# Kernel tuning notes

Hardware: AMD Instinct MI355X
Metric: run time of the kernel (lower is better)

The kernel has to match this reference:

```python
import jax, jax.numpy as jnp
import numpy as np

VOCAB, X, H, C_CLS = 32000, 300, 512, 5
B, N_LEAVES = 256, 256  # complete binary trees, depth 9, 511 nodes/tree

def setup_inputs() -> dict:
    key = jax.random.key(0)
    ks = jax.random.split(key, 10)
    s = lambda k, shp, fan: jax.random.normal(k, shp, jnp.float32) * (1.0 / np.sqrt(fan))
    return {
        'wordid': jax.random.randint(ks[0], (B, N_LEAVES), 0, VOCAB),
        'emb': jax.random.normal(ks[1], (VOCAB, X), jnp.float32) * 0.1,
        'W_iou_w': s(ks[2], (3 * H, X), X),
        'W_iou_b': jnp.zeros((3 * H,), jnp.float32),
        'U_iou_w': s(ks[3], (3 * H, 2 * H), 2 * H),
        'U_iou_b': jnp.zeros((3 * H,), jnp.float32),
        'U_f_w': s(ks[4], (2 * H, 2 * H), 2 * H),
        'U_f_b': jnp.zeros((2 * H,), jnp.float32),
        'lin_w': s(ks[5], (C_CLS, H), H),
        'lin_b': jnp.zeros((C_CLS,), jnp.float32),
    }

def _cell(iou, c_f):
    i, o, u = jnp.split(iou, 3, axis=-1)
    c = jax.nn.sigmoid(i) * jnp.tanh(u) + c_f
    h = jax.nn.sigmoid(o) * jnp.tanh(c)
    return h, c

def reference(wordid, emb, W_iou_w, W_iou_b, U_iou_w, U_iou_b, U_f_w, U_f_b, lin_w, lin_b):
    b, n = wordid.shape
    # leaves: is_leaf=1 -> iou = W_iou(x), c_f = 0
    x = emb[wordid]                                   # [B, L, X]
    iou = x @ W_iou_w.T + W_iou_b                     # [B, L, 3H]
    h, c = _cell(iou, 0.0)
    hs = [h]
    # internal levels: reduce over exactly 2 children (binary TreeLSTM)
    while h.shape[1] > 1:
        m = h.shape[1] // 2
        h_cat = h.reshape(b, m, 2 * H)                # concat of 2 children
        c_pair = c.reshape(b, m, 2, H)
        f = jax.nn.sigmoid(h_cat @ U_f_w.T + U_f_b).reshape(b, m, 2, H)
        c_f = jnp.sum(f * c_pair, axis=2)             # [B, m, H]
        iou = h_cat @ U_iou_w.T + U_iou_b             # is_leaf=0 branch
        h, c = _cell(iou, c_f)
        hs.append(h)
    h_all = jnp.concatenate(hs, axis=1)               # [B, 2L-1, H], leaves-first topo order
    # dropout is identity at inference
    logits = h_all @ lin_w.T + lin_b                  # [B, 2L-1, num_classes]
    return logits
```

## Files before the change

kernel.cpp:

```cpp
#include <hip/hip_runtime.h>
#include <hip/hip_bf16.h>


typedef __bf16 bf16;
typedef bf16  bf16x8 __attribute__((ext_vector_type(8)));
typedef float f32x4  __attribute__((ext_vector_type(4)));

__device__ __forceinline__ float sigm(float x){ return 1.0f/(1.0f + __expf(-x)); }
__device__ __forceinline__ float tanh_f(float x){ return 1.0f - 2.0f/(__expf(2.0f*x)+1.0f); }

__device__ __forceinline__ void gload16(const bf16* g, bf16* l){
  __builtin_amdgcn_global_load_lds(
      (const __attribute__((address_space(1))) void*)g,
      (__attribute__((address_space(3))) void*)l, 16, 0, 0);
}

#define FENCE_VM(N) do{ asm volatile("s_waitcnt vmcnt(" #N ")" ::: "memory"); \
  __builtin_amdgcn_sched_barrier(0); __builtin_amdgcn_s_barrier(); \
  __builtin_amdgcn_sched_barrier(0); }while(0)
#define FENCE_LGKM do{ asm volatile("s_waitcnt lgkmcnt(0)" ::: "memory"); \
  __builtin_amdgcn_sched_barrier(0); __builtin_amdgcn_s_barrier(); \
  __builtin_amdgcn_sched_barrier(0); }while(0)

__global__ void cvt_all(const float* __restrict__ Wiou, const float* __restrict__ Uiou,
                        const float* __restrict__ Uf, const float* __restrict__ emb,
                        bf16* __restrict__ Wpad, bf16* __restrict__ Uall,
                        bf16* __restrict__ embp){
  const long long gid = (long long)blockIdx.x*256 + threadIdx.x;
  const long long NW = 122880, NE = 2560000, NU = 655360;
  if (gid < NW + NE){
    long long g = gid;
    const float* src; bf16* dst;
    if (g < NW){ src = Wiou; dst = Wpad; }
    else       { g -= NW; src = emb; dst = embp; }
    const int r = (int)(g / 80), v = (int)(g % 80);
    bf16 o0, o1, o2, o3;
    if (v < 75){
      const f32x4 x = *(const f32x4*)(src + (size_t)r*300 + v*4);
      o0=(bf16)x[0]; o1=(bf16)x[1]; o2=(bf16)x[2]; o3=(bf16)x[3];
    } else {
      o0=o1=o2=o3=(bf16)0.f;
    }
    bf16* d = dst + (size_t)r*320 + v*4;
    d[0]=o0; d[1]=o1; d[2]=o2; d[3]=o3;
  } else {
    const long long i4 = gid - NW - NE;
    if (i4 < NU){
      const size_t i = (size_t)i4*4;
      const float* s = (i < (size_t)1536*1024) ? (Uiou + i)
                                               : (Uf + (i - (size_t)1536*1024));
      const f32x4 x = *(const f32x4*)s;
      bf16* d = Uall + i;
      d[0]=(bf16)x[0]; d[1]=(bf16)x[1]; d[2]=(bf16)x[2]; d[3]=(bf16)x[3];
    }
  }
}

__global__ __launch_bounds__(256, 2)
void leaf128_kernel(const int* __restrict__ wordid, const bf16* __restrict__ embp,
                    const bf16* __restrict__ Wpad, const float* __restrict__ Wb,
                    bf16* __restrict__ hcur, float* __restrict__ ccur)
{
  __shared__ bf16 lsA[2][128*32];
  __shared__ bf16 lsB[2][192*32];
  const int t = threadIdx.x;
  const int mrow0 = blockIdx.x*128, nblk = blockIdx.y*64;
  const int lane16 = t&15, quad = (t&63)>>4, w = t>>6;

  const int lrow = t>>2;
  const int qsw  = ((t&3) ^ ((t>>3)&3))*8;
  const int wb   = (t & 192)*8;

  const int wid0 = wordid[mrow0 + lrow];
  const int wid1 = wordid[mrow0 + 64 + lrow];
  const bf16* srcA0 = embp + (size_t)wid0*320 + qsw;
  const bf16* srcA1 = embp + (size_t)wid1*320 + qsw;
  const bf16* srcB0 = Wpad + (size_t)(0*512 + nblk + lrow)*320 + qsw;
  const bf16* srcB1 = Wpad + (size_t)(1*512 + nblk + lrow)*320 + qsw;
  const bf16* srcB2 = Wpad + (size_t)(2*512 + nblk + lrow)*320 + qsw;

  const int sA   = (t>>1)&3;
  const int aoff = lane16*32 + ((quad ^ sA)*8);
  const int boff = (w*16 + lane16)*32 + ((quad ^ sA)*8);

  f32x4 acc[3][8];
  const f32x4 zero = {0.f,0.f,0.f,0.f};
  #pragma unroll
  for(int o=0;o<3;o++){
    #pragma unroll
    for(int rt=0;rt<8;rt++) acc[o][rt]=zero;
  }

  {
    gload16(srcA0     , lsA[0] + wb);        gload16(srcA1     , lsA[0] + 2048 + wb);
    gload16(srcB0     , lsB[0] + wb);        gload16(srcB1     , lsB[0] + 2048 + wb);
    gload16(srcB2     , lsB[0] + 4096 + wb);
    gload16(srcA0 + 32, lsA[1] + wb);        gload16(srcA1 + 32, lsA[1] + 2048 + wb);
    gload16(srcB0 + 32, lsB[1] + wb);        gload16(srcB1 + 32, lsB[1] + 2048 + wb);
    gload16(srcB2 + 32, lsB[1] + 4096 + wb);
  }
  FENCE_VM(5);

  for (int ks = 0; ks < 10; ks++){
    const int cur = ks & 1;
    bf16x8 bfrag[3], afrag[8];
    #pragma unroll
    for(int g=0;g<3;g++) bfrag[g] = *(const bf16x8*)&lsB[cur][g*2048 + boff];
    #pragma unroll
    for(int rt=0;rt<8;rt++) afrag[rt] = *(const bf16x8*)&lsA[cur][rt*512 + aoff];
    FENCE_LGKM;
    if (ks < 8){
      const int k0 = (ks+2)*32;
      gload16(srcA0 + k0, lsA[cur] + wb);        gload16(srcA1 + k0, lsA[cur] + 2048 + wb);
      gload16(srcB0 + k0, lsB[cur] + wb);        gload16(srcB1 + k0, lsB[cur] + 2048 + wb);
      gload16(srcB2 + k0, lsB[cur] + 4096 + wb);
    }
    __builtin_amdgcn_s_setprio(1);
    #pragma unroll
    for(int rt=0;rt<8;rt++){
      #pragma unroll
      for(int g=0;g<3;g++)
        acc[g][rt] = __builtin_amdgcn_mfma_f32_16x16x32_bf16(afrag[rt], bfrag[g], acc[g][rt], 0,0,0);
    }
    __builtin_amdgcn_s_setprio(0);
    if (ks < 8)      FENCE_VM(5);
    else if (ks < 9) FENCE_VM(0);
  }
  const int j = nblk + w*16 + lane16;
  const float bi=Wb[j], bo=Wb[512+j], bu=Wb[1024+j];
  #pragma unroll
  for(int rt=0;rt<8;rt++){
    #pragma unroll
    for(int reg=0;reg<4;reg++){
      const int row = mrow0 + rt*16 + quad*4 + reg;
      float iv=acc[0][rt][reg]+bi, ov=acc[1][rt][reg]+bo, uv=acc[2][rt][reg]+bu;
      float c = sigm(iv)*tanh_f(uv);
      float h = sigm(ov)*tanh_f(c);
      ccur[(size_t)row*512 + j] = c;
      hcur[(size_t)row*512 + j] = (bf16)h;
    }
  }
}

__global__ __launch_bounds__(256, 3)
void level_kernel(const bf16* __restrict__ hprev, bf16* __restrict__ hcur,
                  const float* __restrict__ cprev, float* __restrict__ ccur,
                  const bf16* __restrict__ Uall, const float* __restrict__ Uioub,
                  const float* __restrict__ Ufb)
{
  __shared__ bf16 lsA[2][64*32];
  __shared__ bf16 lsB[2][320*32];
  const int t = threadIdx.x;
  const int mrow0 = blockIdx.x*64, nblk = blockIdx.y*64;
  const int lane16 = t&15, quad = (t&63)>>4, w = t>>6;

  const int lrow = t>>2;
  const int qsw  = ((t&3) ^ ((t>>3)&3))*8;
  const int wb   = (t & 192)*8;

  const bf16* srcA0 = hprev + (size_t)(mrow0 + lrow)*1024 + qsw;
  const bf16* srcB0 = Uall + (size_t)(0*512 + nblk + lrow)*1024 + qsw;
  const bf16* srcB1 = Uall + (size_t)(1*512 + nblk + lrow)*1024 + qsw;
  const bf16* srcB2 = Uall + (size_t)(2*512 + nblk + lrow)*1024 + qsw;
  const bf16* srcB3 = Uall + (size_t)(3*512 + nblk + lrow)*1024 + qsw;
  const bf16* srcB4 = Uall + (size_t)(4*512 + nblk + lrow)*1024 + qsw;

  const int sA   = (t>>1)&3;
  const int aoff = lane16*32 + ((quad ^ sA)*8);
  const int boff = (w*16 + lane16)*32 + ((quad ^ sA)*8);

#define LV64_DMA(buf, k0) do{ \
  gload16(srcA0 + (k0), lsA[buf] + wb); \
  gload16(srcB0 + (k0), lsB[buf] + wb);        gload16(srcB1 + (k0), lsB[buf] + 2048 + wb); \
  gload16(srcB2 + (k0), lsB[buf] + 4096 + wb); gload16(srcB3 + (k0), lsB[buf] + 6144 + wb); \
  gload16(srcB4 + (k0), lsB[buf] + 8192 + wb); }while(0)

  f32x4 acc[5][4];
  const f32x4 zero = {0.f,0.f,0.f,0.f};
  #pragma unroll
  for(int o=0;o<5;o++){
    #pragma unroll
    for(int rt=0;rt<4;rt++) acc[o][rt]=zero;
  }

  LV64_DMA(0, 0); LV64_DMA(1, 32);
  FENCE_VM(6);

  for (int ks = 0; ks < 32; ks++){
    const int cur = ks & 1;
    bf16x8 bfrag[5], afrag[4];
    #pragma unroll
    for(int g=0;g<5;g++) bfrag[g] = *(const bf16x8*)&lsB[cur][g*2048 + boff];
    #pragma unroll
    for(int rt=0;rt<4;rt++) afrag[rt] = *(const bf16x8*)&lsA[cur][rt*512 + aoff];
    FENCE_LGKM;
    if (ks < 30){
      LV64_DMA(cur, (ks+2)*32);
    }
    __builtin_amdgcn_s_setprio(1);
    #pragma unroll
    for(int rt=0;rt<4;rt++){
      #pragma unroll
      for(int g=0;g<5;g++)
        acc[g][rt] = __builtin_amdgcn_mfma_f32_16x16x32_bf16(afrag[rt], bfrag[g], acc[g][rt], 0,0,0);
    }
    __builtin_amdgcn_s_setprio(0);
    if (ks < 30)       FENCE_VM(6);
    else if (ks < 31)  FENCE_VM(0);
  }

  const int j = nblk + w*16 + lane16;
  const float bi =Uioub[j], bo=Uioub[512+j], bu=Uioub[1024+j];
  const float bfl=Ufb[j],   bfr=Ufb[512+j];
  #pragma unroll
  for(int rt=0;rt<4;rt++){
    #pragma unroll
    for(int reg=0;reg<4;reg++){
      const int row = mrow0 + rt*16 + quad*4 + reg;
      float iv=acc[0][rt][reg]+bi, ov=acc[1][rt][reg]+bo, uv=acc[2][rt][reg]+bu;
      float fl=acc[3][rt][reg]+bfl, fr=acc[4][rt][reg]+bfr;
      float cl = cprev[((size_t)row*2  )*512 + j];
      float cr = cprev[((size_t)row*2+1)*512 + j];
      float cf = sigm(fl)*cl + sigm(fr)*cr;
      float c  = sigm(iv)*tanh_f(uv) + cf;
      float h  = sigm(ov)*tanh_f(c);
      ccur[(size_t)row*512 + j] = c;
      hcur[(size_t)row*512 + j] = (bf16)h;
    }
  }
#undef LV64_DMA
}

__global__ __launch_bounds__(256, 2)
void level128_kernel(const bf16* __restrict__ hprev, bf16* __restrict__ hcur,
                     const float* __restrict__ cprev, float* __restrict__ ccur,
                     const bf16* __restrict__ Uall, const float* __restrict__ Uioub,
                     const float* __restrict__ Ufb)
{
  __shared__ bf16 lsA[128*32];
  __shared__ bf16 lsB[2][320*32];
  const int t = threadIdx.x;
  const int mrow0 = blockIdx.x*128, nblk = blockIdx.y*64;
  const int lane16 = t&15, quad = (t&63)>>4, w = t>>6;

  const int lrow = t>>2;
  const int qsw  = ((t&3) ^ ((t>>3)&3))*8;
  const int wb   = (t & 192)*8;

  const bf16* srcA0 = hprev + (size_t)(mrow0 + lrow)*1024 + qsw;
  const bf16* srcA1 = hprev + (size_t)(mrow0 + 64 + lrow)*1024 + qsw;
  const bf16* srcB0 = Uall + (size_t)(0*512 + nblk + lrow)*1024 + qsw;
  const bf16* srcB1 = Uall + (size_t)(1*512 + nblk + lrow)*1024 + qsw;
  const bf16* srcB2 = Uall + (size_t)(2*512 + nblk + lrow)*1024 + qsw;
  const bf16* srcB3 = Uall + (size_t)(3*512 + nblk + lrow)*1024 + qsw;
  const bf16* srcB4 = Uall + (size_t)(4*512 + nblk + lrow)*1024 + qsw;

  const int sA   = (t>>1)&3;
  const int aoff = lane16*32 + ((quad ^ sA)*8);
  const int boff = (w*16 + lane16)*32 + ((quad ^ sA)*8);

#define LVL_DMA_A(k0) do{ \
  gload16(srcA0 + (k0), lsA + wb);             gload16(srcA1 + (k0), lsA + 2048 + wb); }while(0)
#define LVL_DMA_B(buf, k0) do{ \
  gload16(srcB0 + (k0), lsB[buf] + wb);        gload16(srcB1 + (k0), lsB[buf] + 2048 + wb); \
  gload16(srcB2 + (k0), lsB[buf] + 4096 + wb); gload16(srcB3 + (k0), lsB[buf] + 6144 + wb); \
  gload16(srcB4 + (k0), lsB[buf] + 8192 + wb); }while(0)

  f32x4 acc[5][8];
  const f32x4 zero = {0.f,0.f,0.f,0.f};
  #pragma unroll
  for(int o=0;o<5;o++){
    #pragma unroll
    for(int rt=0;rt<8;rt++) acc[o][rt]=zero;
  }

  LVL_DMA_A(0); LVL_DMA_B(0, 0);
  LVL_DMA_B(1, 32);
  FENCE_VM(5);

  for (int ks = 0; ks < 32; ks++){
    const int cur = ks & 1;
    bf16x8 bfrag[5], afrag[8];
    #pragma unroll
    for(int g=0;g<5;g++) bfrag[g] = *(const bf16x8*)&lsB[cur][g*2048 + boff];
    #pragma unroll
    for(int rt=0;rt<8;rt++) afrag[rt] = *(const bf16x8*)&lsA[rt*512 + aoff];
    FENCE_LGKM;
    if (ks < 31) LVL_DMA_A(ks*32 + 32);
    if (ks < 30) LVL_DMA_B(cur, (ks+2)*32);
    __builtin_amdgcn_s_setprio(1);
    #pragma unroll
    for(int rt=0;rt<8;rt++){
      #pragma unroll
      for(int g=0;g<5;g++)
        acc[g][rt] = __builtin_amdgcn_mfma_f32_16x16x32_bf16(afrag[rt], bfrag[g], acc[g][rt], 0,0,0);
    }
    __builtin_amdgcn_s_setprio(0);
    if (ks < 30)       FENCE_VM(5);
    else if (ks < 31)  FENCE_VM(0);
  }

  const int j = nblk + w*16 + lane16;
  const float bi =Uioub[j], bo=Uioub[512+j], bu=Uioub[1024+j];
  const float bfl=Ufb[j],   bfr=Ufb[512+j];
  #pragma unroll
  for(int rt=0;rt<8;rt++){
    #pragma unroll
    for(int reg=0;reg<4;reg++){
      const int row = mrow0 + rt*16 + quad*4 + reg;
      float iv=acc[0][rt][reg]+bi, ov=acc[1][rt][reg]+bo, uv=acc[2][rt][reg]+bu;
      float fl=acc[3][rt][reg]+bfl, fr=acc[4][rt][reg]+bfr;
      float cl = cprev[((size_t)row*2  )*512 + j];
      float cr = cprev[((size_t)row*2+1)*512 + j];
      float cf = sigm(fl)*cl + sigm(fr)*cr;
      float c  = sigm(iv)*tanh_f(uv) + cf;
      float h  = sigm(ov)*tanh_f(c);
      ccur[(size_t)row*512 + j] = c;
      hcur[(size_t)row*512 + j] = (bf16)h;
    }
  }
#undef LVL_DMA_A
#undef LVL_DMA_B
}

__global__ __launch_bounds__(256)
void logits_kernel(const bf16* __restrict__ h, const float* __restrict__ linw,
                   const float* __restrict__ linb, float* __restrict__ out,
                   int rowbase, int lgm, int mask, int off){
  const int row = blockIdx.x*4 + (threadIdx.x>>6);
  const int l = threadIdx.x & 63;
  bf16x8 hv = *(const bf16x8*)(h + (size_t)row*512 + l*8);
  float hf[8];
  #pragma unroll
  for(int jj=0;jj<8;jj++) hf[jj] = (float)hv[jj];
  float s[5];
  #pragma unroll
  for(int c=0;c<5;c++){
    const f32x4 w0 = *(const f32x4*)(linw + c*512 + l*8);
    const f32x4 w1 = *(const f32x4*)(linw + c*512 + l*8 + 4);
    float a = 0.f;
    #pragma unroll
    for(int jj=0;jj<4;jj++) a += hf[jj]*w0[jj] + hf[4+jj]*w1[jj];
    s[c]=a;
  }
  #pragma unroll
  for(int o=32;o>0;o>>=1){
    #pragma unroll
    for(int c=0;c<5;c++) s[c] += __shfl_down(s[c], o, 64);
  }
  if (l==0){
    const int g = rowbase + row;
    const int node = (g>>lgm)*511 + off + (g&mask);
    #pragma unroll
    for(int c=0;c<5;c++) out[(size_t)node*5+c] = s[c] + linb[c];
  }
}

__global__ __launch_bounds__(256)
void logits2_kernel(const bf16* __restrict__ ha, int rows_a, int lgm_a, int mask_a, int off_a,
                    const bf16* __restrict__ hb, int lgm_b, int mask_b, int off_b,
                    const float* __restrict__ linw, const float* __restrict__ linb,
                    float* __restrict__ out){
  const int row = blockIdx.x*4 + (threadIdx.x>>6);
  const int l = threadIdx.x & 63;
  const bf16* hrow; int g, lgm, mask, off;
  if (row < rows_a){ hrow = ha + (size_t)row*512;            g = row;           lgm=lgm_a; mask=mask_a; off=off_a; }
  else             { hrow = hb + (size_t)(row-rows_a)*512;   g = row - rows_a;  lgm=lgm_b; mask=mask_b; off=off_b; }
  bf16x8 hv = *(const bf16x8*)(hrow + l*8);
  float hf[8];
  #pragma unroll
  for(int jj=0;jj<8;jj++) hf[jj] = (float)hv[jj];
  float s[5];
  #pragma unroll
  for(int c=0;c<5;c++){
    const f32x4 w0 = *(const f32x4*)(linw + c*512 + l*8);
    const f32x4 w1 = *(const f32x4*)(linw + c*512 + l*8 + 4);
    float a = 0.f;
    #pragma unroll
    for(int jj=0;jj<4;jj++) a += hf[jj]*w0[jj] + hf[4+jj]*w1[jj];
    s[c]=a;
  }
  #pragma unroll
  for(int o=32;o>0;o>>=1){
    #pragma unroll
    for(int c=0;c<5;c++) s[c] += __shfl_down(s[c], o, 64);
  }
  if (l==0){
    const int node = (g>>lgm)*511 + off + (g&mask);
    #pragma unroll
    for(int c=0;c<5;c++) out[(size_t)node*5+c] = s[c] + linb[c];
  }
}

__global__ void zero_out(float* out, int n){
  int i = blockIdx.x*256 + threadIdx.x;
  if (i < n) out[i] = 0.f;
}

extern "C" void kernel_launch(void* const* d_in, const int* in_sizes, int n_in,
                              void* d_out, int out_size, void* d_ws, size_t ws_size,
                              hipStream_t stream)
{
  const int*   wordid = (const int*)d_in[0];
  const float* emb    = (const float*)d_in[1];
  const float* Wiou   = (const float*)d_in[2];
  const float* Wioub  = (const float*)d_in[3];
  const float* Uiou   = (const float*)d_in[4];
  const float* Uioub  = (const float*)d_in[5];
  const float* Uf     = (const float*)d_in[6];
  const float* Ufb    = (const float*)d_in[7];
  const float* linw   = (const float*)d_in[8];
  const float* linb   = (const float*)d_in[9];
  float* out = (float*)d_out;

  const size_t oWPD  = 0;
  const size_t oUALL = oWPD  + (size_t)1536*320*2;
  const size_t oEMB  = oUALL + (size_t)2560*1024*2;
  const size_t oH1   = oEMB  + (size_t)32000*320*2;
  const size_t oC1   = oH1   + (size_t)32768*512*2;
  const size_t oH0   = oC1   + (size_t)32768*512*4;
  size_t R0 = 0;
  {
    const size_t t2 = oH0 + (size_t)32768*512*(2+4);
    const size_t t4 = oH0 + (size_t)16384*512*(2+4);
    const size_t t8 = oH0 + (size_t) 8192*512*(2+4);
    if      (ws_size >= t2) R0 = 32768;
    else if (ws_size >= t4) R0 = 16384;
    else if (ws_size >= t8) R0 = 8192;
  }
  if (R0 == 0){
    zero_out<<<(out_size+255)/256, 256, 0, stream>>>(out, out_size);
    return;
  }

  char* ws = (char*)d_ws;
  bf16*  Wpad = (bf16*)(ws + oWPD);
  bf16*  Uall = (bf16*)(ws + oUALL);
  bf16*  embp = (bf16*)(ws + oEMB);
  bf16*  h1   = (bf16*)(ws + oH1);
  float* c1   = (float*)(ws + oC1);
  bf16*  h0   = (bf16*)(ws + oH0);
  float* c0   = (float*)(ws + oH0 + R0*1024);

  cvt_all<<<13040, 256, 0, stream>>>(Wiou, Uiou, Uf, emb, Wpad, Uall, embp);

  const int offs[9] = {0,256,384,448,480,496,504,508,510};
  const int nchunk = (int)(65536 / R0);

  for (int ch = 0; ch < nchunk; ch++){
    const int* wid = wordid + (size_t)ch*R0;
    leaf128_kernel<<<dim3((int)(R0/128), 8), 256, 0, stream>>>(wid, embp, Wpad, Wioub,
                                                               h0, c0);
    logits_kernel<<<(int)(R0/4), 256, 0, stream>>>(h0, linw, linb, out,
                                                   (int)(ch*R0), 8, 255, 0);
    bf16*  h1c = h1 + (size_t)ch*(R0/2)*512;
    float* c1c = c1 + (size_t)ch*(R0/2)*512;
    const int orows = (int)(R0/2);
    level128_kernel<<<dim3(orows/128, 8), 256, 0, stream>>>(h0, h1c, c0, c1c,
                                                            Uall, Uioub, Ufb);
  }

  for (int lv = 2; lv <= 8; lv++){
    const int rows = 65536 >> lv;
    const bf16*  hin  = (lv & 1) ? h0 : h1;
    bf16*        hout = (lv & 1) ? h1 : h0;
    const float* cin  = (lv & 1) ? c0 : c1;
    float*       cout = (lv & 1) ? c1 : c0;
    if (rows >= 8192)
      level128_kernel<<<dim3(rows/128, 8), 256, 0, stream>>>(hin, hout, cin, cout,
                                                             Uall, Uioub, Ufb);
    else
      level_kernel<<<dim3(rows/64, 8), 256, 0, stream>>>(hin, hout, cin, cout,
                                                         Uall, Uioub, Ufb);
    if ((lv & 1) == 0){
      const int rows_a = 65536 >> (lv-1);
      const int rows_b = rows;
      logits2_kernel<<<(rows_a + rows_b)/4, 256, 0, stream>>>(
          h1, rows_a, 8-(lv-1), (256>>(lv-1))-1, offs[lv-1],
          h0,         8-lv,     (256>>lv)-1,     offs[lv],
          linw, linb, out);
    }
  }
}
```

Before: 763.0 us.

## Enlarge level GEMM tile to 256 rows with 512-thread blocks sharing B

Replaces the 128-row, 256-thread level kernel with a 256-row, 512-thread variant. Eight waves are arranged as two row halves by four column groups, so each staged U-weight tile in LDS is reused across twice as many output rows. This halves weight traffic per output and reduces the DMA issue count per thread. The gate-4 slice is loaded redundantly by both thread halves. Occupancy drops to one block per CU (64KB LDS), and the chunked level-1 launch now falls back to the small kernel when there are fewer than 8192 rows.

Measured after the change: 759.3 us (median of 2 runs). About the same (-0.5%).

```diff
diff --git a/kernel.cpp b/kernel.cpp
--- a/kernel.cpp
+++ b/kernel.cpp
@@ -231,40 +231,43 @@
 #undef LV64_DMA
 }
 
-__global__ __launch_bounds__(256, 2)
-void level128_kernel(const bf16* __restrict__ hprev, bf16* __restrict__ hcur,
+__global__ __launch_bounds__(512, 1)
+void level256_kernel(const bf16* __restrict__ hprev, bf16* __restrict__ hcur,
                      const float* __restrict__ cprev, float* __restrict__ ccur,
                      const bf16* __restrict__ Uall, const float* __restrict__ Uioub,
                      const float* __restrict__ Ufb)
 {
-  __shared__ bf16 lsA[128*32];
-  __shared__ bf16 lsB[2][320*32];
+  __shared__ bf16 lsA[256*32];
+  __shared__ bf16 lsB[2][6*2048];
   const int t = threadIdx.x;
-  const int mrow0 = blockIdx.x*128, nblk = blockIdx.y*64;
-  const int lane16 = t&15, quad = (t&63)>>4, w = t>>6;
-
-  const int lrow = t>>2;
+  const int mrow0 = blockIdx.x*256, nblk = blockIdx.y*64;
+  const int lane16 = t&15, quad = (t&63)>>4;
+  const int wc = (t>>6)&3;
+  const int wh = t>>8;
+
   const int qsw  = ((t&3) ^ ((t>>3)&3))*8;
-  const int wb   = (t & 192)*8;
-
-  const bf16* srcA0 = hprev + (size_t)(mrow0 + lrow)*1024 + qsw;
-  const bf16* srcA1 = hprev + (size_t)(mrow0 + 64 + lrow)*1024 + qsw;
-  const bf16* srcB0 = Uall + (size_t)(0*512 + nblk + lrow)*1024 + qsw;
-  const bf16* srcB1 = Uall + (size_t)(1*512 + nblk + lrow)*1024 + qsw;
-  const bf16* srcB2 = Uall + (size_t)(2*512 + nblk + lrow)*1024 + qsw;
-  const bf16* srcB3 = Uall + (size_t)(3*512 + nblk + lrow)*1024 + qsw;
-  const bf16* srcB4 = Uall + (size_t)(4*512 + nblk + lrow)*1024 + qsw;
+  const int wb   = (t & 448)*8;
+
+  const int arow = t>>2;
+  const bf16* srcA_lo = hprev + (size_t)(mrow0 +       arow)*1024 + qsw;
+  const bf16* srcA_hi = hprev + (size_t)(mrow0 + 128 + arow)*1024 + qsw;
+  const int brow  = (t&255)>>2;
+  const int bhalf = t>>8;
+  const bf16* srcB01 = Uall + (size_t)((0+bhalf)*512 + nblk + brow)*1024 + qsw;
+  const bf16* srcB23 = Uall + (size_t)((2+bhalf)*512 + nblk + brow)*1024 + qsw;
+  const bf16* srcB4  = Uall + (size_t)(4*512         + nblk + brow)*1024 + qsw;
 
   const int sA   = (t>>1)&3;
-  const int aoff = lane16*32 + ((quad ^ sA)*8);
-  const int boff = (w*16 + lane16)*32 + ((quad ^ sA)*8);
-
-#define LVL_DMA_A(k0) do{ \
-  gload16(srcA0 + (k0), lsA + wb);             gload16(srcA1 + (k0), lsA + 2048 + wb); }while(0)
-#define LVL_DMA_B(buf, k0) do{ \
-  gload16(srcB0 + (k0), lsB[buf] + wb);        gload16(srcB1 + (k0), lsB[buf] + 2048 + wb); \
-  gload16(srcB2 + (k0), lsB[buf] + 4096 + wb); gload16(srcB3 + (k0), lsB[buf] + 6144 + wb); \
-  gload16(srcB4 + (k0), lsB[buf] + 8192 + wb); }while(0)
+  const int aoff = (wh*128 + lane16)*32 + ((quad ^ sA)*8);
+  const int boff = (wc*16 + lane16)*32 + ((quad ^ sA)*8);
+
+#define LV256_DMA_A(k0) do{ \
+  gload16(srcA_lo + (k0), lsA + wb); \
+  gload16(srcA_hi + (k0), lsA + 4096 + wb); }while(0)
+#define LV256_DMA_B(buf, k0) do{ \
+  gload16(srcB01 + (k0), lsB[buf] + wb); \
+  gload16(srcB23 + (k0), lsB[buf] + 4096 + wb); \
+  gload16(srcB4  + (k0), lsB[buf] + 8192 + wb); }while(0)
 
   f32x4 acc[5][8];
   const f32x4 zero = {0.f,0.f,0.f,0.f};
@@ -274,9 +277,9 @@
     for(int rt=0;rt<8;rt++) acc[o][rt]=zero;
   }
 
-  LVL_DMA_A(0); LVL_DMA_B(0, 0);
-  LVL_DMA_B(1, 32);
-  FENCE_VM(5);
+  LV256_DMA_A(0); LV256_DMA_B(0, 0);
+  LV256_DMA_B(1, 32);
+  FENCE_VM(3);
 
   for (int ks = 0; ks < 32; ks++){
     const int cur = ks & 1;
@@ -286,8 +289,8 @@
     #pragma unroll
     for(int rt=0;rt<8;rt++) afrag[rt] = *(const bf16x8*)&lsA[rt*512 + aoff];
     FENCE_LGKM;
-    if (ks < 31) LVL_DMA_A(ks*32 + 32);
-    if (ks < 30) LVL_DMA_B(cur, (ks+2)*32);
+    if (ks < 31) LV256_DMA_A((ks+1)*32);
+    if (ks < 30) LV256_DMA_B(cur, (ks+2)*32);
     __builtin_amdgcn_s_setprio(1);
     #pragma unroll
     for(int rt=0;rt<8;rt++){
@@ -296,18 +299,18 @@
         acc[g][rt] = __builtin_amdgcn_mfma_f32_16x16x32_bf16(afrag[rt], bfrag[g], acc[g][rt], 0,0,0);
     }
     __builtin_amdgcn_s_setprio(0);
-    if (ks < 30)       FENCE_VM(5);
+    if (ks < 30)       FENCE_VM(3);
     else if (ks < 31)  FENCE_VM(0);
   }
 
-  const int j = nblk + w*16 + lane16;
+  const int j = nblk + wc*16 + lane16;
   const float bi =Uioub[j], bo=Uioub[512+j], bu=Uioub[1024+j];
   const float bfl=Ufb[j],   bfr=Ufb[512+j];
   #pragma unroll
   for(int rt=0;rt<8;rt++){
     #pragma unroll
     for(int reg=0;reg<4;reg++){
-      const int row = mrow0 + rt*16 + quad*4 + reg;
+      const int row = mrow0 + wh*128 + rt*16 + quad*4 + reg;
       float iv=acc[0][rt][reg]+bi, ov=acc[1][rt][reg]+bo, uv=acc[2][rt][reg]+bu;
       float fl=acc[3][rt][reg]+bfl, fr=acc[4][rt][reg]+bfr;
       float cl = cprev[((size_t)row*2  )*512 + j];
@@ -319,8 +322,8 @@
       hcur[(size_t)row*512 + j] = (bf16)h;
     }
   }
-#undef LVL_DMA_A
-#undef LVL_DMA_B
+#undef LV256_DMA_A
+#undef LV256_DMA_B
 }
 
 __global__ __launch_bounds__(256)
@@ -456,8 +459,12 @@
     bf16*  h1c = h1 + (size_t)ch*(R0/2)*512;
     float* c1c = c1 + (size_t)ch*(R0/2)*512;
     const int orows = (int)(R0/2);
-    level128_kernel<<<dim3(orows/128, 8), 256, 0, stream>>>(h0, h1c, c0, c1c,
-                                                            Uall, Uioub, Ufb);
+    if (orows >= 8192)
+      level256_kernel<<<dim3(orows/256, 8), 512, 0, stream>>>(h0, h1c, c0, c1c,
+                                                              Uall, Uioub, Ufb);
+    else
+      level_kernel<<<dim3(orows/64, 8), 256, 0, stream>>>(h0, h1c, c0, c1c,
+                                                          Uall, Uioub, Ufb);
   }
 
   for (int lv = 2; lv <= 8; lv++){
@@ -467,7 +474,7 @@
     const float* cin  = (lv & 1) ? c0 : c1;
     float*       cout = (lv & 1) ? c1 : c0;
     if (rows >= 8192)
-      level128_kernel<<<dim3(rows/128, 8), 256, 0, stream>>>(hin, hout, cin, cout,
+      level256_kernel<<<dim3(rows/256, 8), 512, 0, stream>>>(hin, hout, cin, cout,
                                                              Uall, Uioub, Ufb);
     else
       level_kernel<<<dim3(rows/64, 8), 256, 0, stream>>>(hin, hout, cin, cout,
```
